# Performance work log

Measured on AMD Instinct MI355X. Metric: run time of the kernel, lower is better.

## Reference

```python
import jax, jax.numpy as jnp
import numpy as np

HEAD_SIZE = 64
INPUT_SIZE = 1024
B, T = 8, 2048


def setup_inputs() -> dict:
    key = jax.random.key(0)
    kx, kq, kk, kv = jax.random.split(key, 4)
    x = jax.random.normal(kx, (B, T, INPUT_SIZE), dtype=jnp.float32)
    s = 1.0 / np.sqrt(INPUT_SIZE)
    Wq = jax.random.uniform(kq, (INPUT_SIZE, HEAD_SIZE), minval=-s, maxval=s, dtype=jnp.float32)
    Wk = jax.random.uniform(kk, (INPUT_SIZE, HEAD_SIZE), minval=-s, maxval=s, dtype=jnp.float32)
    Wv = jax.random.uniform(kv, (INPUT_SIZE, HEAD_SIZE), minval=-s, maxval=s, dtype=jnp.float32)
    return {"x": x, "Wq": Wq, "Wk": Wk, "Wv": Wv}


def reference(x, Wq, Wk, Wv):
    # Faithful to the torch module: scores = K @ Q^T (note: keys times queries^T),
    # causal mask on upper triangle of that matrix, softmax over last axis,
    # dropout treated as identity (eval), then scores @ V.
    q = jnp.einsum('bti,ih->bth', x, Wq)  # [B,T,H]
    k = jnp.einsum('bti,ih->bth', x, Wk)
    v = jnp.einsum('bti,ih->bth', x, Wv)
    scale = HEAD_SIZE ** -0.5
    scores = jnp.einsum('bth,bsh->bts', k, q) * scale  # [B,T,T] = K Q^T
    Tlen = x.shape[1]
    causal = jnp.tril(jnp.ones((Tlen, Tlen), dtype=bool))
    scores = jnp.where(causal, scores, -jnp.inf)
    w = jax.nn.softmax(scores, axis=-1)
    out = jnp.einsum('bts,bsh->bth', w, v)  # [B,T,H]
    return out
```

## Files before the change

### kernel.cpp

```cpp
#include <hip/hip_runtime.h>

typedef __bf16 bf16_t;
typedef bf16_t bf16x8 __attribute__((ext_vector_type(8)));
typedef float f32x4 __attribute__((ext_vector_type(4)));

#define NB 8
#define TT 2048
#define DIN 1024
#define HH 64
#define MM (NB * TT)

__device__ __forceinline__ unsigned short f2bf(float f) {
    unsigned int u = __float_as_uint(f);
    u += 0x7fffu + ((u >> 16) & 1u);
    return (unsigned short)(u >> 16);
}

__device__ __forceinline__ void async16(void* l, const void* g) {
    __builtin_amdgcn_global_load_lds(
        (const __attribute__((address_space(1))) unsigned int*)g,
        (__attribute__((address_space(3))) unsigned int*)l, 16, 0, 0);
}

__device__ __forceinline__ int block_detect_f32(const unsigned int* __restrict__ xw,
                                                int tid, int* sflag) {
    if (tid < 64) {
        unsigned int u = xw[tid];
        unsigned int e = (u >> 7) & 0xFFu;
        unsigned long long m = __ballot(e >= 100u && e <= 150u);
        if (tid == 0) *sflag = (__popcll(m) < 48) ? 1 : 0;
    }
    __syncthreads();
    return *sflag;
}

__global__ __launch_bounds__(256) void transpose_w_kernel(
    const void* __restrict__ Wq, const void* __restrict__ Wk,
    const void* __restrict__ Wv, const unsigned int* __restrict__ xw,
    unsigned short* __restrict__ Wt) {
    __shared__ int sflag;
    __shared__ unsigned short ts[64][68];
    const int tid = threadIdx.x;
    const int isf32 = block_detect_f32(xw, tid, &sflag);
    const int w = blockIdx.x >> 4, kt = blockIdx.x & 15;
    const void* W = (w == 0) ? Wq : (w == 1) ? Wk : Wv;
    const int kk = tid >> 4, nn = (tid & 15) * 4;
#pragma unroll
    for (int j = 0; j < 4; ++j) {
        int k = kk + j * 16;
        if (isf32) {
            float4 f = *(const float4*)((const float*)W + (size_t)(kt * 64 + k) * 64 + nn);
            ts[k][nn + 0] = f2bf(f.x); ts[k][nn + 1] = f2bf(f.y);
            ts[k][nn + 2] = f2bf(f.z); ts[k][nn + 3] = f2bf(f.w);
        } else {
            *(uint2*)&ts[k][nn] =
                *(const uint2*)((const unsigned short*)W + (size_t)(kt * 64 + k) * 64 + nn);
        }
    }
    __syncthreads();
    const int n = tid >> 2, k0 = (tid & 3) * 16;
    unsigned short tmp[16];
#pragma unroll
    for (int j = 0; j < 16; ++j) tmp[j] = ts[k0 + j][n];
    unsigned short* dst = Wt + (size_t)(w * 64 + n) * 1024 + kt * 64 + k0;
    *(uint4*)(dst + 0) = *(uint4*)&tmp[0];
    *(uint4*)(dst + 8) = *(uint4*)&tmp[8];
}

#define XR 72
#define WROWC 9
#define PN 48

__global__ __launch_bounds__(256, 2) void proj_kernel(
    const void* __restrict__ xraw, const unsigned short* __restrict__ Wt,
    unsigned short* __restrict__ qbuf, unsigned short* __restrict__ kbuf,
    unsigned short* __restrict__ vtbuf) {
    __shared__ int sflag;
    __shared__ __align__(16) unsigned short xs[64 * XR];
    __shared__ __align__(16) unsigned char wlds[PN * WROWC * 16];

    const int tid = threadIdx.x;
    const int isf32 = block_detect_f32((const unsigned int*)xraw, tid, &sflag);
    const int m0 = blockIdx.x * 64;
    const int nh = blockIdx.y;
    const int wave = tid >> 6, lane = tid & 63, quad = lane >> 4, l15 = lane & 15;

    const float* xf = (const float*)xraw;
    const unsigned short* xb = (const unsigned short*)xraw;
    const unsigned char* wg = (const unsigned char*)Wt;

    const unsigned char* wsrc[2];
    unsigned int wdst[2];
    int nw = 0;
#pragma unroll
    for (int j = 0; j < 2; ++j) {
        int c = (wave + 4 * j) * 64 + lane;
        if (c < PN * WROWC) {
            int R = c / WROWC, cc = c % WROWC;
            int ccu = (cc > 7) ? 0 : cc;
            wsrc[nw] = wg + (size_t)(nh * PN + R) * 2048 + ccu * 16;
            wdst[nw] = c * 16;
            ++nw;
        }
    }

    const int xr = tid >> 2, xc = (tid & 3) * 16;
    float4 px[4];
    uint4  pxb[2];
    auto ldx = [&](int k0) {
        if (isf32) {
            const float* g = xf + (size_t)(m0 + xr) * DIN + k0 + xc;
#pragma unroll
            for (int j = 0; j < 4; ++j) px[j] = *(const float4*)(g + j * 4);
        } else {
            const unsigned short* g = xb + (size_t)(m0 + xr) * DIN + k0 + xc;
            pxb[0] = *(const uint4*)(g + 0);
            pxb[1] = *(const uint4*)(g + 8);
        }
    };

    f32x4 acc[3];
#pragma unroll
    for (int ct = 0; ct < 3; ++ct) acc[ct] = (f32x4){0.f, 0.f, 0.f, 0.f};

    ldx(0);
    size_t woff = 0;
    for (int it = 0; it < 16; ++it) {
        __syncthreads();
        if (isf32) {
            unsigned short t[16];
#pragma unroll
            for (int j = 0; j < 4; ++j) {
                t[j * 4 + 0] = f2bf(px[j].x); t[j * 4 + 1] = f2bf(px[j].y);
                t[j * 4 + 2] = f2bf(px[j].z); t[j * 4 + 3] = f2bf(px[j].w);
            }
            *(uint4*)&xs[xr * XR + xc + 0] = *(uint4*)&t[0];
            *(uint4*)&xs[xr * XR + xc + 8] = *(uint4*)&t[8];
        } else {
            *(uint4*)&xs[xr * XR + xc + 0] = pxb[0];
            *(uint4*)&xs[xr * XR + xc + 8] = pxb[1];
        }
        for (int j = 0; j < nw; ++j) async16(&wlds[wdst[j]], wsrc[j] + woff);
        woff += 128;
        __syncthreads();

        if (it < 15) ldx((it + 1) * 64);

#pragma unroll
        for (int ks = 0; ks < 2; ++ks) {
            bf16x8 a = *(const bf16x8*)&xs[(wave * 16 + l15) * XR + ks * 32 + quad * 8];
            bf16x8 b[3];
#pragma unroll
            for (int ct = 0; ct < 3; ++ct)
                b[ct] = *(const bf16x8*)
                    &wlds[(ct * 16 + l15) * (WROWC * 16) + ks * 64 + quad * 16];
#pragma unroll
            for (int ct = 0; ct < 3; ++ct)
                acc[ct] = __builtin_amdgcn_mfma_f32_16x16x32_bf16(
                    a, b[ct], acc[ct], 0, 0, 0);
        }
    }

#pragma unroll
    for (int ct = 0; ct < 3; ++ct) {
        int n = nh * PN + ct * 16 + l15;
        int wsel = n >> 6, nn = n & 63;
#pragma unroll
        for (int reg = 0; reg < 4; ++reg) {
            int m = m0 + wave * 16 + quad * 4 + reg;
            unsigned short bv = f2bf(acc[ct][reg]);
            if (wsel == 0)      qbuf[(size_t)m * HH + nn] = bv;
            else if (wsel == 1) kbuf[(size_t)m * HH + nn] = bv;
            else {
                int bb = m >> 11, t = m & 2047;
                vtbuf[((size_t)bb * HH + nn) * TT + t] = bv;
            }
        }
    }
}

__global__ __launch_bounds__(256, 4) void attn_kernel(
    const unsigned short* __restrict__ rowbuf,
    const unsigned short* __restrict__ colbuf,
    const unsigned short* __restrict__ vtbuf,
    float* __restrict__ O_part,
    float* __restrict__ l_part) {

    __shared__ __align__(16) unsigned short Qr_s[64][72];
    __shared__ __align__(16) unsigned short Kc_s[64][72];
    __shared__ __align__(16) unsigned short Vt_s[64][72];
    __shared__ __align__(16) unsigned short P_s[4][16][72];

    const int tid  = threadIdx.x;
    const int bid  = blockIdx.x;
    const int b    = bid & 7;
    const int bx   = bid >> 3;
    int rt, ch;
    if (bx < 8)       { rt = bx;                 ch = 0; }
    else if (bx < 24) { rt = 8 + ((bx - 8) >> 1);  ch = (bx - 8) & 1; }
    else if (bx < 48) { rt = 16 + (bx - 24) / 3;   ch = (bx - 24) % 3; }
    else              { rt = 24 + ((bx - 48) >> 2); ch = (bx - 48) & 3; }
    const int nct = min(8, rt + 1 - ch * 8);
    const int t0 = rt * 64;
    const int slot = b * 80 + bx;

    const int wave = tid >> 6, lane = tid & 63, quad = lane >> 4, l15 = lane & 15;
    const int sr = tid >> 2, sc = (tid & 3) * 16;

    {
        const uint4* g = (const uint4*)(rowbuf + ((size_t)b * TT + t0 + sr) * HH + sc);
        *(uint4*)&Qr_s[sr][sc + 0] = g[0];
        *(uint4*)&Qr_s[sr][sc + 8] = g[1];
    }

    f32x4 o[4];
#pragma unroll
    for (int c = 0; c < 4; ++c) o[c] = (f32x4){0.f, 0.f, 0.f, 0.f};
    float ls[4] = {0.f, 0.f, 0.f, 0.f};

    const float SCL2 = 0.125f * 1.4426950408889634f;

    uint4 pk0, pk1, pv0, pv1;
    auto loadKV = [&](int i) {
        const int s0 = (ch * 8 + i) * 64;
        const uint4* gk = (const uint4*)(colbuf + ((size_t)b * TT + s0 + sr) * HH + sc);
        pk0 = gk[0]; pk1 = gk[1];
        const uint4* gv = (const uint4*)(vtbuf + ((size_t)b * HH + sr) * TT + s0 + sc);
        pv0 = gv[0]; pv1 = gv[1];
    };
    loadKV(0);

    for (int i = 0; i < nct; ++i) {
        const int stc = ch * 8 + i;
        const int s0 = stc * 64;
        *(uint4*)&Kc_s[sr][sc + 0] = pk0;
        *(uint4*)&Kc_s[sr][sc + 8] = pk1;
        *(uint4*)&Vt_s[sr][sc + 0] = pv0;
        *(uint4*)&Vt_s[sr][sc + 8] = pv1;
        __syncthreads();

        f32x4 scf[4];
#pragma unroll
        for (int c = 0; c < 4; ++c) scf[c] = (f32x4){0.f, 0.f, 0.f, 0.f};
        __builtin_amdgcn_s_setprio(1);
#pragma unroll
        for (int ks = 0; ks < 2; ++ks) {
            bf16x8 a = *(const bf16x8*)&Qr_s[wave * 16 + l15][ks * 32 + quad * 8];
#pragma unroll
            for (int c = 0; c < 4; ++c) {
                bf16x8 bb = *(const bf16x8*)&Kc_s[c * 16 + l15][ks * 32 + quad * 8];
                scf[c] = __builtin_amdgcn_mfma_f32_16x16x32_bf16(a, bb, scf[c], 0, 0, 0);
            }
        }
        __builtin_amdgcn_s_setprio(0);

        if (i + 1 < nct) loadKV(i + 1);

        const bool diag = (stc == rt);
#pragma unroll
        for (int r = 0; r < 4; ++r) {
            const int tg = t0 + wave * 16 + quad * 4 + r;
#pragma unroll
            for (int c = 0; c < 4; ++c) {
                float arg = fmaf(scf[c][r], SCL2, -30.f);
                if (diag && (s0 + c * 16 + l15) > tg) arg = -200.f;
                float p = __builtin_amdgcn_exp2f(arg);
                P_s[wave][quad * 4 + r][c * 16 + l15] = f2bf(p);
                ls[r] += p;
            }
        }
        __builtin_amdgcn_s_setprio(1);
#pragma unroll
        for (int ks = 0; ks < 2; ++ks) {
            bf16x8 ap = *(const bf16x8*)&P_s[wave][l15][ks * 32 + quad * 8];
#pragma unroll
            for (int c = 0; c < 4; ++c) {
                bf16x8 bv = *(const bf16x8*)&Vt_s[c * 16 + l15][ks * 32 + quad * 8];
                o[c] = __builtin_amdgcn_mfma_f32_16x16x32_bf16(ap, bv, o[c], 0, 0, 0);
            }
        }
        __builtin_amdgcn_s_setprio(0);
        __syncthreads();
    }

#pragma unroll
    for (int r = 0; r < 4; ++r) {
#pragma unroll
        for (int off = 1; off < 16; off <<= 1) ls[r] += __shfl_xor(ls[r], off);
    }
    if (l15 == 0) {
#pragma unroll
        for (int r = 0; r < 4; ++r)
            l_part[(size_t)slot * 64 + wave * 16 + quad * 4 + r] = ls[r];
    }
#pragma unroll
    for (int c = 0; c < 4; ++c)
#pragma unroll
        for (int r = 0; r < 4; ++r)
            O_part[(size_t)slot * 4096 + (wave * 16 + quad * 4 + r) * 64 + c * 16 + l15] = o[c][r];
}

__global__ __launch_bounds__(256) void combine_kernel(
    const float* __restrict__ O_part, const float* __restrict__ l_part,
    const unsigned int* __restrict__ xw, void* __restrict__ outraw) {
    __shared__ int sflag;
    const int tid = threadIdx.x;
    const int isf32 = block_detect_f32(xw, tid, &sflag);
    const int bid = blockIdx.x;
    const int b = bid & 7, rt = bid >> 3;
    const int nch = rt / 8 + 1;
    const int off = (rt < 8) ? rt : (rt < 16) ? 8 + 2 * (rt - 8)
                   : (rt < 24) ? 24 + 3 * (rt - 16) : 48 + 4 * (rt - 24);
    const int slot0 = b * 80 + off;

    const int row = tid >> 2, cb = (tid & 3) * 16;
    f32x4 a[4];
#pragma unroll
    for (int q = 0; q < 4; ++q) a[q] = (f32x4){0.f, 0.f, 0.f, 0.f};
    float l = 0.f;
    for (int j = 0; j < nch; ++j) {
        const f32x4* p = (const f32x4*)(O_part + (size_t)(slot0 + j) * 4096 + row * 64 + cb);
#pragma unroll
        for (int q = 0; q < 4; ++q) a[q] += p[q];
        l += l_part[(size_t)(slot0 + j) * 64 + row];
    }
    const float inv = 1.f / l;
    const size_t base = ((size_t)b * TT + rt * 64 + row) * HH + cb;
    if (isf32) {
        float* outf = (float*)outraw;
#pragma unroll
        for (int q = 0; q < 4; ++q) {
            f32x4 v = a[q] * inv;
            *(f32x4*)(outf + base + q * 4) = v;
        }
    } else {
        unsigned short h[16];
#pragma unroll
        for (int q = 0; q < 4; ++q)
#pragma unroll
            for (int e = 0; e < 4; ++e) h[q * 4 + e] = f2bf(a[q][e] * inv);
        unsigned short* outb = (unsigned short*)outraw;
        *(uint4*)(outb + base + 0) = *(uint4*)&h[0];
        *(uint4*)(outb + base + 8) = *(uint4*)&h[8];
    }
}

extern "C" void kernel_launch(void* const* d_in, const int* in_sizes, int n_in,
                              void* d_out, int out_size, void* d_ws, size_t ws_size,
                              hipStream_t stream) {
    const void* x  = d_in[0];
    const void* Wq = d_in[1];
    const void* Wk = d_in[2];
    const void* Wv = d_in[3];
    unsigned short* ws = (unsigned short*)d_ws;

    unsigned short* qbuf  = ws;
    unsigned short* kbuf  = ws + (size_t)MM * HH;
    unsigned short* vtbuf = ws + (size_t)2 * MM * HH;
    unsigned short* wtbuf = ws + (size_t)3 * MM * HH;
    float* O_part = (float*)(ws + (size_t)3 * MM * HH + 3 * 65536);
    float* l_part = O_part + (size_t)640 * 4096;

    hipLaunchKernelGGL(transpose_w_kernel, dim3(48), dim3(256), 0, stream,
                       Wq, Wk, Wv, (const unsigned int*)x, wtbuf);
    hipLaunchKernelGGL(proj_kernel, dim3(256, 4), dim3(256), 0, stream,
                       x, wtbuf, qbuf, kbuf, vtbuf);
    hipLaunchKernelGGL(attn_kernel, dim3(640), dim3(256), 0, stream,
                       kbuf, qbuf, vtbuf, O_part, l_part);
    hipLaunchKernelGGL(combine_kernel, dim3(256), dim3(256), 0, stream,
                       O_part, l_part, (const unsigned int*)x, d_out);
}
```

Baseline: 144.7 us.

## Drop LDS staging in projection and attention, load MFMA operands from global

The projection kernel now reads x and transposed weights straight from global memory into MFMA operand registers, with no LDS tiles or barriers. The attention kernel keeps its row block in registers and reads column-side and V tiles directly from global/L2 per wave, dropping shared tiles and __syncthreads. The key chunk size per block falls from 8 to 4, giving 1152 split blocks instead of 640 for better load balance, with more partials for the combine step. The cost is redundant global/L2 traffic across waves, uncoalesced strided loads, and no explicit prefetch overlap.

```diff
diff --git a/kernel.cpp b/kernel.cpp
--- a/kernel.cpp
+++ b/kernel.cpp
@@ -2,6 +2,7 @@
 
 typedef __bf16 bf16_t;
 typedef bf16_t bf16x8 __attribute__((ext_vector_type(8)));
+typedef unsigned short u16x8 __attribute__((ext_vector_type(8)));
 typedef float f32x4 __attribute__((ext_vector_type(4)));
 
 #define NB 8
@@ -10,16 +11,14 @@
 #define HH 64
 #define MM (NB * TT)
 
+#define CHUNK 4
+#define BPB 144
+#define NSLOT (NB * BPB)
+
 __device__ __forceinline__ unsigned short f2bf(float f) {
     unsigned int u = __float_as_uint(f);
     u += 0x7fffu + ((u >> 16) & 1u);
     return (unsigned short)(u >> 16);
-}
-
-__device__ __forceinline__ void async16(void* l, const void* g) {
-    __builtin_amdgcn_global_load_lds(
-        (const __attribute__((address_space(1))) unsigned int*)g,
-        (__attribute__((address_space(3))) unsigned int*)l, 16, 0, 0);
 }
 
 __device__ __forceinline__ int block_detect_f32(const unsigned int* __restrict__ xw,
@@ -67,97 +66,61 @@
     *(uint4*)(dst + 8) = *(uint4*)&tmp[8];
 }
 
-#define XR 72
-#define WROWC 9
 #define PN 48
 
-__global__ __launch_bounds__(256, 2) void proj_kernel(
+__global__ __launch_bounds__(256) void proj_kernel(
     const void* __restrict__ xraw, const unsigned short* __restrict__ Wt,
     unsigned short* __restrict__ qbuf, unsigned short* __restrict__ kbuf,
     unsigned short* __restrict__ vtbuf) {
     __shared__ int sflag;
-    __shared__ __align__(16) unsigned short xs[64 * XR];
-    __shared__ __align__(16) unsigned char wlds[PN * WROWC * 16];
-
     const int tid = threadIdx.x;
     const int isf32 = block_detect_f32((const unsigned int*)xraw, tid, &sflag);
     const int m0 = blockIdx.x * 64;
     const int nh = blockIdx.y;
     const int wave = tid >> 6, lane = tid & 63, quad = lane >> 4, l15 = lane & 15;
 
-    const float* xf = (const float*)xraw;
-    const unsigned short* xb = (const unsigned short*)xraw;
+    const int row = m0 + wave * 16 + l15;
+    const float* xrow = (const float*)xraw + (size_t)row * DIN;
+    const unsigned short* xrowb = (const unsigned short*)xraw + (size_t)row * DIN;
+
     const unsigned char* wg = (const unsigned char*)Wt;
-
-    const unsigned char* wsrc[2];
-    unsigned int wdst[2];
-    int nw = 0;
-#pragma unroll
-    for (int j = 0; j < 2; ++j) {
-        int c = (wave + 4 * j) * 64 + lane;
-        if (c < PN * WROWC) {
-            int R = c / WROWC, cc = c % WROWC;
-            int ccu = (cc > 7) ? 0 : cc;
-            wsrc[nw] = wg + (size_t)(nh * PN + R) * 2048 + ccu * 16;
-            wdst[nw] = c * 16;
-            ++nw;
-        }
-    }
-
-    const int xr = tid >> 2, xc = (tid & 3) * 16;
-    float4 px[4];
-    uint4  pxb[2];
-    auto ldx = [&](int k0) {
-        if (isf32) {
-            const float* g = xf + (size_t)(m0 + xr) * DIN + k0 + xc;
-#pragma unroll
-            for (int j = 0; j < 4; ++j) px[j] = *(const float4*)(g + j * 4);
-        } else {
-            const unsigned short* g = xb + (size_t)(m0 + xr) * DIN + k0 + xc;
-            pxb[0] = *(const uint4*)(g + 0);
-            pxb[1] = *(const uint4*)(g + 8);
-        }
-    };
+    const unsigned char* wrow0 = wg + (size_t)(nh * PN +  0 + l15) * 2048 + quad * 16;
+    const unsigned char* wrow1 = wg + (size_t)(nh * PN + 16 + l15) * 2048 + quad * 16;
+    const unsigned char* wrow2 = wg + (size_t)(nh * PN + 32 + l15) * 2048 + quad * 16;
 
     f32x4 acc[3];
 #pragma unroll
     for (int ct = 0; ct < 3; ++ct) acc[ct] = (f32x4){0.f, 0.f, 0.f, 0.f};
 
-    ldx(0);
-    size_t woff = 0;
-    for (int it = 0; it < 16; ++it) {
-        __syncthreads();
-        if (isf32) {
-            unsigned short t[16];
-#pragma unroll
-            for (int j = 0; j < 4; ++j) {
-                t[j * 4 + 0] = f2bf(px[j].x); t[j * 4 + 1] = f2bf(px[j].y);
-                t[j * 4 + 2] = f2bf(px[j].z); t[j * 4 + 3] = f2bf(px[j].w);
-            }
-            *(uint4*)&xs[xr * XR + xc + 0] = *(uint4*)&t[0];
-            *(uint4*)&xs[xr * XR + xc + 8] = *(uint4*)&t[8];
-        } else {
-            *(uint4*)&xs[xr * XR + xc + 0] = pxb[0];
-            *(uint4*)&xs[xr * XR + xc + 8] = pxb[1];
-        }
-        for (int j = 0; j < nw; ++j) async16(&wlds[wdst[j]], wsrc[j] + woff);
-        woff += 128;
-        __syncthreads();
-
-        if (it < 15) ldx((it + 1) * 64);
-
-#pragma unroll
-        for (int ks = 0; ks < 2; ++ks) {
-            bf16x8 a = *(const bf16x8*)&xs[(wave * 16 + l15) * XR + ks * 32 + quad * 8];
-            bf16x8 b[3];
-#pragma unroll
-            for (int ct = 0; ct < 3; ++ct)
-                b[ct] = *(const bf16x8*)
-                    &wlds[(ct * 16 + l15) * (WROWC * 16) + ks * 64 + quad * 16];
-#pragma unroll
-            for (int ct = 0; ct < 3; ++ct)
-                acc[ct] = __builtin_amdgcn_mfma_f32_16x16x32_bf16(
-                    a, b[ct], acc[ct], 0, 0, 0);
+    if (isf32) {
+#pragma unroll 4
+        for (int kk = 0; kk < 32; ++kk) {
+            const int c0 = kk * 32 + quad * 8;
+            float4 f0 = *(const float4*)(xrow + c0);
+            float4 f1 = *(const float4*)(xrow + c0 + 4);
+            bf16x8 a;
+            a[0] = (bf16_t)f0.x; a[1] = (bf16_t)f0.y;
+            a[2] = (bf16_t)f0.z; a[3] = (bf16_t)f0.w;
+            a[4] = (bf16_t)f1.x; a[5] = (bf16_t)f1.y;
+            a[6] = (bf16_t)f1.z; a[7] = (bf16_t)f1.w;
+            bf16x8 b0 = *(const bf16x8*)(wrow0 + kk * 64);
+            bf16x8 b1 = *(const bf16x8*)(wrow1 + kk * 64);
+            bf16x8 b2 = *(const bf16x8*)(wrow2 + kk * 64);
+            acc[0] = __builtin_amdgcn_mfma_f32_16x16x32_bf16(a, b0, acc[0], 0, 0, 0);
+            acc[1] = __builtin_amdgcn_mfma_f32_16x16x32_bf16(a, b1, acc[1], 0, 0, 0);
+            acc[2] = __builtin_amdgcn_mfma_f32_16x16x32_bf16(a, b2, acc[2], 0, 0, 0);
+        }
+    } else {
+#pragma unroll 4
+        for (int kk = 0; kk < 32; ++kk) {
+            const int c0 = kk * 32 + quad * 8;
+            bf16x8 a = *(const bf16x8*)(xrowb + c0);
+            bf16x8 b0 = *(const bf16x8*)(wrow0 + kk * 64);
+            bf16x8 b1 = *(const bf16x8*)(wrow1 + kk * 64);
+            bf16x8 b2 = *(const bf16x8*)(wrow2 + kk * 64);
+            acc[0] = __builtin_amdgcn_mfma_f32_16x16x32_bf16(a, b0, acc[0], 0, 0, 0);
+            acc[1] = __builtin_amdgcn_mfma_f32_16x16x32_bf16(a, b1, acc[1], 0, 0, 0);
+            acc[2] = __builtin_amdgcn_mfma_f32_16x16x32_bf16(a, b2, acc[2], 0, 0, 0);
         }
     }
 
@@ -179,39 +142,39 @@
     }
 }
 
-__global__ __launch_bounds__(256, 4) void attn_kernel(
+__global__ __launch_bounds__(256) void attn_kernel(
     const unsigned short* __restrict__ rowbuf,
     const unsigned short* __restrict__ colbuf,
     const unsigned short* __restrict__ vtbuf,
     float* __restrict__ O_part,
     float* __restrict__ l_part) {
 
-    __shared__ __align__(16) unsigned short Qr_s[64][72];
-    __shared__ __align__(16) unsigned short Kc_s[64][72];
-    __shared__ __align__(16) unsigned short Vt_s[64][72];
     __shared__ __align__(16) unsigned short P_s[4][16][72];
 
     const int tid  = threadIdx.x;
     const int bid  = blockIdx.x;
     const int b    = bid & 7;
     const int bx   = bid >> 3;
-    int rt, ch;
-    if (bx < 8)       { rt = bx;                 ch = 0; }
-    else if (bx < 24) { rt = 8 + ((bx - 8) >> 1);  ch = (bx - 8) & 1; }
-    else if (bx < 48) { rt = 16 + (bx - 24) / 3;   ch = (bx - 24) % 3; }
-    else              { rt = 24 + ((bx - 48) >> 2); ch = (bx - 48) & 3; }
-    const int nct = min(8, rt + 1 - ch * 8);
+    int rt = 0, ch = 0;
+    {
+        int a = 0;
+        for (int r = 0; r < 32; ++r) {
+            int nc = (r + CHUNK) >> 2;
+            if (bx < a + nc) { rt = r; ch = bx - a; break; }
+            a += nc;
+        }
+    }
+    const int nct = min(CHUNK, rt + 1 - ch * CHUNK);
     const int t0 = rt * 64;
-    const int slot = b * 80 + bx;
+    const int slot = b * BPB + bx;
 
     const int wave = tid >> 6, lane = tid & 63, quad = lane >> 4, l15 = lane & 15;
-    const int sr = tid >> 2, sc = (tid & 3) * 16;
-
-    {
-        const uint4* g = (const uint4*)(rowbuf + ((size_t)b * TT + t0 + sr) * HH + sc);
-        *(uint4*)&Qr_s[sr][sc + 0] = g[0];
-        *(uint4*)&Qr_s[sr][sc + 8] = g[1];
-    }
+
+    bf16x8 aq[2];
+#pragma unroll
+    for (int ks = 0; ks < 2; ++ks)
+        aq[ks] = *(const bf16x8*)(rowbuf +
+            ((size_t)b * TT + t0 + wave * 16 + l15) * HH + ks * 32 + quad * 8);
 
     f32x4 o[4];
 #pragma unroll
@@ -220,24 +183,12 @@
 
     const float SCL2 = 0.125f * 1.4426950408889634f;
 
-    uint4 pk0, pk1, pv0, pv1;
-    auto loadKV = [&](int i) {
-        const int s0 = (ch * 8 + i) * 64;
-        const uint4* gk = (const uint4*)(colbuf + ((size_t)b * TT + s0 + sr) * HH + sc);
-        pk0 = gk[0]; pk1 = gk[1];
-        const uint4* gv = (const uint4*)(vtbuf + ((size_t)b * HH + sr) * TT + s0 + sc);
-        pv0 = gv[0]; pv1 = gv[1];
-    };
-    loadKV(0);
+    const unsigned short* qb = colbuf + (size_t)b * TT * HH;
+    const unsigned short* vb = vtbuf + (size_t)b * HH * TT;
 
     for (int i = 0; i < nct; ++i) {
-        const int stc = ch * 8 + i;
+        const int stc = ch * CHUNK + i;
         const int s0 = stc * 64;
-        *(uint4*)&Kc_s[sr][sc + 0] = pk0;
-        *(uint4*)&Kc_s[sr][sc + 8] = pk1;
-        *(uint4*)&Vt_s[sr][sc + 0] = pv0;
-        *(uint4*)&Vt_s[sr][sc + 8] = pv1;
-        __syncthreads();
 
         f32x4 scf[4];
 #pragma unroll
@@ -245,16 +196,14 @@
         __builtin_amdgcn_s_setprio(1);
 #pragma unroll
         for (int ks = 0; ks < 2; ++ks) {
-            bf16x8 a = *(const bf16x8*)&Qr_s[wave * 16 + l15][ks * 32 + quad * 8];
 #pragma unroll
             for (int c = 0; c < 4; ++c) {
-                bf16x8 bb = *(const bf16x8*)&Kc_s[c * 16 + l15][ks * 32 + quad * 8];
-                scf[c] = __builtin_amdgcn_mfma_f32_16x16x32_bf16(a, bb, scf[c], 0, 0, 0);
+                bf16x8 bq = *(const bf16x8*)(qb +
+                    (size_t)(s0 + c * 16 + l15) * HH + ks * 32 + quad * 8);
+                scf[c] = __builtin_amdgcn_mfma_f32_16x16x32_bf16(aq[ks], bq, scf[c], 0, 0, 0);
             }
         }
         __builtin_amdgcn_s_setprio(0);
-
-        if (i + 1 < nct) loadKV(i + 1);
 
         const bool diag = (stc == rt);
 #pragma unroll
@@ -275,12 +224,12 @@
             bf16x8 ap = *(const bf16x8*)&P_s[wave][l15][ks * 32 + quad * 8];
 #pragma unroll
             for (int c = 0; c < 4; ++c) {
-                bf16x8 bv = *(const bf16x8*)&Vt_s[c * 16 + l15][ks * 32 + quad * 8];
+                bf16x8 bv = *(const bf16x8*)(vb +
+                    (size_t)(c * 16 + l15) * TT + s0 + ks * 32 + quad * 8);
                 o[c] = __builtin_amdgcn_mfma_f32_16x16x32_bf16(ap, bv, o[c], 0, 0, 0);
             }
         }
         __builtin_amdgcn_s_setprio(0);
-        __syncthreads();
     }
 
 #pragma unroll
@@ -308,10 +257,10 @@
     const int isf32 = block_detect_f32(xw, tid, &sflag);
     const int bid = blockIdx.x;
     const int b = bid & 7, rt = bid >> 3;
-    const int nch = rt / 8 + 1;
-    const int off = (rt < 8) ? rt : (rt < 16) ? 8 + 2 * (rt - 8)
-                   : (rt < 24) ? 24 + 3 * (rt - 16) : 48 + 4 * (rt - 24);
-    const int slot0 = b * 80 + off;
+    const int nch = (rt + CHUNK) >> 2;
+    int off = 0;
+    for (int r = 0; r < rt; ++r) off += (r + CHUNK) >> 2;
+    const int slot0 = b * BPB + off;
 
     const int row = tid >> 2, cb = (tid & 3) * 16;
     f32x4 a[4];
@@ -359,13 +308,13 @@
     unsigned short* vtbuf = ws + (size_t)2 * MM * HH;
     unsigned short* wtbuf = ws + (size_t)3 * MM * HH;
     float* O_part = (float*)(ws + (size_t)3 * MM * HH + 3 * 65536);
-    float* l_part = O_part + (size_t)640 * 4096;
+    float* l_part = O_part + (size_t)NSLOT * 4096;
 
     hipLaunchKernelGGL(transpose_w_kernel, dim3(48), dim3(256), 0, stream,
                        Wq, Wk, Wv, (const unsigned int*)x, wtbuf);
     hipLaunchKernelGGL(proj_kernel, dim3(256, 4), dim3(256), 0, stream,
                        x, wtbuf, qbuf, kbuf, vtbuf);
-    hipLaunchKernelGGL(attn_kernel, dim3(640), dim3(256), 0, stream,
+    hipLaunchKernelGGL(attn_kernel, dim3(NSLOT), dim3(256), 0, stream,
                        kbuf, qbuf, vtbuf, O_part, l_part);
     hipLaunchKernelGGL(combine_kernel, dim3(256), dim3(256), 0, stream,
                        O_part, l_part, (const unsigned int*)x, d_out);
```

New measurement: 208.5 us. +44.1%, slower.

## Halve attention split-K chunk size and double projection K-tile depth

Applied to the files above, without the earlier changes.

The attention kernel now splits each row tile's causal key range into chunks of 4 key tiles instead of 8, growing the grid from 640 to 1152 blocks for finer load balance and more parallelism. The combine kernel's slot indexing is regenerated with a loop to match. Separately, the projection kernel processes 128-wide K slices per iteration (8 iterations instead of 16), which halves the barrier count at the cost of more LDS and registers. The trade-off is more partial-output traffic and combine work.

```diff
diff --git a/kernel.cpp b/kernel.cpp
--- a/kernel.cpp
+++ b/kernel.cpp
@@ -9,6 +9,10 @@
 #define DIN 1024
 #define HH 64
 #define MM (NB * TT)
+
+#define CHUNK 4
+#define BPB 144
+#define NSLOT (NB * BPB)
 
 __device__ __forceinline__ unsigned short f2bf(float f) {
     unsigned int u = __float_as_uint(f);
@@ -67,17 +71,17 @@
     *(uint4*)(dst + 8) = *(uint4*)&tmp[8];
 }
 
-#define XR 72
-#define WROWC 9
 #define PN 48
+#define XR2 136
+#define WCH 17
 
 __global__ __launch_bounds__(256, 2) void proj_kernel(
     const void* __restrict__ xraw, const unsigned short* __restrict__ Wt,
     unsigned short* __restrict__ qbuf, unsigned short* __restrict__ kbuf,
     unsigned short* __restrict__ vtbuf) {
     __shared__ int sflag;
-    __shared__ __align__(16) unsigned short xs[64 * XR];
-    __shared__ __align__(16) unsigned char wlds[PN * WROWC * 16];
+    __shared__ __align__(16) unsigned short xs[64 * XR2];
+    __shared__ __align__(16) unsigned char wlds[PN * WCH * 16];
 
     const int tid = threadIdx.x;
     const int isf32 = block_detect_f32((const unsigned int*)xraw, tid, &sflag);
@@ -89,33 +93,33 @@
     const unsigned short* xb = (const unsigned short*)xraw;
     const unsigned char* wg = (const unsigned char*)Wt;
 
-    const unsigned char* wsrc[2];
-    unsigned int wdst[2];
+    const unsigned char* wsrc[4];
+    unsigned int wdst[4];
     int nw = 0;
 #pragma unroll
-    for (int j = 0; j < 2; ++j) {
-        int c = (wave + 4 * j) * 64 + lane;
-        if (c < PN * WROWC) {
-            int R = c / WROWC, cc = c % WROWC;
-            int ccu = (cc > 7) ? 0 : cc;
+    for (int j = 0; j < 4; ++j) {
+        int c = tid + 256 * j;
+        if (c < PN * WCH) {
+            int R = c / WCH, cc = c % WCH;
+            int ccu = (cc > 15) ? 0 : cc;
             wsrc[nw] = wg + (size_t)(nh * PN + R) * 2048 + ccu * 16;
             wdst[nw] = c * 16;
             ++nw;
         }
     }
 
-    const int xr = tid >> 2, xc = (tid & 3) * 16;
-    float4 px[4];
-    uint4  pxb[2];
+    const int xr = tid >> 2, xc = (tid & 3) * 32;
+    float4 px[8];
+    uint4  pxb[4];
     auto ldx = [&](int k0) {
         if (isf32) {
             const float* g = xf + (size_t)(m0 + xr) * DIN + k0 + xc;
 #pragma unroll
-            for (int j = 0; j < 4; ++j) px[j] = *(const float4*)(g + j * 4);
+            for (int j = 0; j < 8; ++j) px[j] = *(const float4*)(g + j * 4);
         } else {
             const unsigned short* g = xb + (size_t)(m0 + xr) * DIN + k0 + xc;
-            pxb[0] = *(const uint4*)(g + 0);
-            pxb[1] = *(const uint4*)(g + 8);
+#pragma unroll
+            for (int j = 0; j < 4; ++j) pxb[j] = *(const uint4*)(g + j * 8);
         }
     };
 
@@ -125,35 +129,37 @@
 
     ldx(0);
     size_t woff = 0;
-    for (int it = 0; it < 16; ++it) {
+    for (int it = 0; it < 8; ++it) {
         __syncthreads();
         if (isf32) {
-            unsigned short t[16];
-#pragma unroll
-            for (int j = 0; j < 4; ++j) {
+            unsigned short t[32];
+#pragma unroll
+            for (int j = 0; j < 8; ++j) {
                 t[j * 4 + 0] = f2bf(px[j].x); t[j * 4 + 1] = f2bf(px[j].y);
                 t[j * 4 + 2] = f2bf(px[j].z); t[j * 4 + 3] = f2bf(px[j].w);
             }
-            *(uint4*)&xs[xr * XR + xc + 0] = *(uint4*)&t[0];
-            *(uint4*)&xs[xr * XR + xc + 8] = *(uint4*)&t[8];
+#pragma unroll
+            for (int j = 0; j < 4; ++j)
+                *(uint4*)&xs[xr * XR2 + xc + j * 8] = *(uint4*)&t[j * 8];
         } else {
-            *(uint4*)&xs[xr * XR + xc + 0] = pxb[0];
-            *(uint4*)&xs[xr * XR + xc + 8] = pxb[1];
+#pragma unroll
+            for (int j = 0; j < 4; ++j)
+                *(uint4*)&xs[xr * XR2 + xc + j * 8] = pxb[j];
         }
         for (int j = 0; j < nw; ++j) async16(&wlds[wdst[j]], wsrc[j] + woff);
-        woff += 128;
+        woff += 256;
         __syncthreads();
 
-        if (it < 15) ldx((it + 1) * 64);
-
-#pragma unroll
-        for (int ks = 0; ks < 2; ++ks) {
-            bf16x8 a = *(const bf16x8*)&xs[(wave * 16 + l15) * XR + ks * 32 + quad * 8];
+        if (it < 7) ldx((it + 1) * 128);
+
+#pragma unroll
+        for (int ks = 0; ks < 4; ++ks) {
+            bf16x8 a = *(const bf16x8*)&xs[(wave * 16 + l15) * XR2 + ks * 32 + quad * 8];
             bf16x8 b[3];
 #pragma unroll
             for (int ct = 0; ct < 3; ++ct)
                 b[ct] = *(const bf16x8*)
-                    &wlds[(ct * 16 + l15) * (WROWC * 16) + ks * 64 + quad * 16];
+                    &wlds[(ct * 16 + l15) * (WCH * 16) + ks * 64 + quad * 16];
 #pragma unroll
             for (int ct = 0; ct < 3; ++ct)
                 acc[ct] = __builtin_amdgcn_mfma_f32_16x16x32_bf16(
@@ -195,14 +201,18 @@
     const int bid  = blockIdx.x;
     const int b    = bid & 7;
     const int bx   = bid >> 3;
-    int rt, ch;
-    if (bx < 8)       { rt = bx;                 ch = 0; }
-    else if (bx < 24) { rt = 8 + ((bx - 8) >> 1);  ch = (bx - 8) & 1; }
-    else if (bx < 48) { rt = 16 + (bx - 24) / 3;   ch = (bx - 24) % 3; }
-    else              { rt = 24 + ((bx - 48) >> 2); ch = (bx - 48) & 3; }
-    const int nct = min(8, rt + 1 - ch * 8);
+    int rt = 0, ch = 0;
+    {
+        int a = 0;
+        for (int r = 0; r < 32; ++r) {
+            int nc = (r + CHUNK) >> 2;
+            if (bx < a + nc) { rt = r; ch = bx - a; break; }
+            a += nc;
+        }
+    }
+    const int nct = min(CHUNK, rt + 1 - ch * CHUNK);
     const int t0 = rt * 64;
-    const int slot = b * 80 + bx;
+    const int slot = b * BPB + bx;
 
     const int wave = tid >> 6, lane = tid & 63, quad = lane >> 4, l15 = lane & 15;
     const int sr = tid >> 2, sc = (tid & 3) * 16;
@@ -222,7 +232,7 @@
 
     uint4 pk0, pk1, pv0, pv1;
     auto loadKV = [&](int i) {
-        const int s0 = (ch * 8 + i) * 64;
+        const int s0 = (ch * CHUNK + i) * 64;
         const uint4* gk = (const uint4*)(colbuf + ((size_t)b * TT + s0 + sr) * HH + sc);
         pk0 = gk[0]; pk1 = gk[1];
         const uint4* gv = (const uint4*)(vtbuf + ((size_t)b * HH + sr) * TT + s0 + sc);
@@ -231,7 +241,7 @@
     loadKV(0);
 
     for (int i = 0; i < nct; ++i) {
-        const int stc = ch * 8 + i;
+        const int stc = ch * CHUNK + i;
         const int s0 = stc * 64;
         *(uint4*)&Kc_s[sr][sc + 0] = pk0;
         *(uint4*)&Kc_s[sr][sc + 8] = pk1;
@@ -308,10 +318,10 @@
     const int isf32 = block_detect_f32(xw, tid, &sflag);
     const int bid = blockIdx.x;
     const int b = bid & 7, rt = bid >> 3;
-    const int nch = rt / 8 + 1;
-    const int off = (rt < 8) ? rt : (rt < 16) ? 8 + 2 * (rt - 8)
-                   : (rt < 24) ? 24 + 3 * (rt - 16) : 48 + 4 * (rt - 24);
-    const int slot0 = b * 80 + off;
+    const int nch = (rt + CHUNK) >> 2;
+    int off = 0;
+    for (int r = 0; r < rt; ++r) off += (r + CHUNK) >> 2;
+    const int slot0 = b * BPB + off;
 
     const int row = tid >> 2, cb = (tid & 3) * 16;
     f32x4 a[4];
@@ -359,13 +369,13 @@
     unsigned short* vtbuf = ws + (size_t)2 * MM * HH;
     unsigned short* wtbuf = ws + (size_t)3 * MM * HH;
     float* O_part = (float*)(ws + (size_t)3 * MM * HH + 3 * 65536);
-    float* l_part = O_part + (size_t)640 * 4096;
+    float* l_part = O_part + (size_t)NSLOT * 4096;
 
     hipLaunchKernelGGL(transpose_w_kernel, dim3(48), dim3(256), 0, stream,
                        Wq, Wk, Wv, (const unsigned int*)x, wtbuf);
     hipLaunchKernelGGL(proj_kernel, dim3(256, 4), dim3(256), 0, stream,
                        x, wtbuf, qbuf, kbuf, vtbuf);
-    hipLaunchKernelGGL(attn_kernel, dim3(640), dim3(256), 0, stream,
+    hipLaunchKernelGGL(attn_kernel, dim3(NSLOT), dim3(256), 0, stream,
                        kbuf, qbuf, vtbuf, O_part, l_part);
     hipLaunchKernelGGL(combine_kernel, dim3(256), dim3(256), 0, stream,
                        O_part, l_part, (const unsigned int*)x, d_out);
```

Result: slower. 153.9 us (+6.4%).
